# Performance work log

Measured on AMD Instinct MI355X. Metric: run time of the kernel, lower is better.

The kernel has to match this reference:

```python
import jax, jax.numpy as jnp
import numpy as np

N_HEADS = 16
SCALE = 0.25  # hard-coded in the torch module


def setup_inputs() -> dict:
    key = jax.random.key(0)
    ks = jax.random.split(key, 5)
    B, S, D = 2, 2048, 1024
    std = 1.0 / np.sqrt(D)
    return {
        "x": jax.random.normal(ks[0], (B, S, D), dtype=jnp.float32),
        "wq": jax.random.normal(ks[1], (D, D), dtype=jnp.float32) * std,
        "wk": jax.random.normal(ks[2], (D, D), dtype=jnp.float32) * std,
        "wv": jax.random.normal(ks[3], (D, D), dtype=jnp.float32) * std,
        "wo": jax.random.normal(ks[4], (D, D), dtype=jnp.float32) * std,
    }


def reference(x, wq, wk, wv, wo):
    B, S, D = x.shape
    H = N_HEADS
    hd = D // H
    # torch Linear(no bias): y = x @ W.T ; weights stored [out, in]
    q = (x @ wq.T).reshape(B, S, H, hd).transpose(0, 2, 1, 3)  # [B,H,S,hd]
    k = (x @ wk.T).reshape(B, S, H, hd).transpose(0, 2, 1, 3)
    v = (x @ wv.T).reshape(B, S, H, hd).transpose(0, 2, 1, 3)

    scores = jnp.einsum("bhqd,bhkd->bhqk", q, k) * SCALE  # [B,H,S,S]
    idx = jnp.arange(S)
    q_idx = idx[:, None]
    kv_idx = idx[None, :]
    # ALiBi-style score_mod: score - |q_idx - kv_idx|
    bias = -jnp.abs(q_idx - kv_idx).astype(scores.dtype)  # [S,S]
    causal = q_idx >= kv_idx  # [S,S]
    scores = jnp.where(causal, scores + bias, -jnp.inf)
    attn = jax.nn.softmax(scores, axis=-1)
    out = jnp.einsum("bhqk,bhkd->bhqd", attn, v)  # [B,H,S,hd]
    out = out.transpose(0, 2, 1, 3).reshape(B, S, D)
    return out @ wo.T
```

## Files before the change

kernel.cpp:

```cpp
#include <hip/hip_runtime.h>
#include <hip/hip_bf16.h>
#include <stdint.h>

typedef __bf16 bf16x8 __attribute__((ext_vector_type(8)));
typedef __bf16 bf16x4 __attribute__((ext_vector_type(4)));
typedef float  f32x4  __attribute__((ext_vector_type(4)));
typedef uint32_t u32x4 __attribute__((ext_vector_type(4)));

#define LOG2E 1.44269504088896f

__device__ __forceinline__ void glds16(const __bf16* g, __bf16* l) {
  __builtin_amdgcn_global_load_lds((const __attribute__((address_space(1))) void*)g,
                                   (__attribute__((address_space(3))) void*)l, 16, 0, 0);
}

__device__ __forceinline__ uint32_t pk2(float lo, float hi) {
  __bf16 l = (__bf16)lo, h = (__bf16)hi;
  uint16_t lb = __builtin_bit_cast(uint16_t, l);
  uint16_t hb = __builtin_bit_cast(uint16_t, h);
  return ((uint32_t)hb << 16) | lb;
}

__global__ __launch_bounds__(256) void cvt_all(
    const float* __restrict__ x,  const float* __restrict__ wq,
    const float* __restrict__ wk, const float* __restrict__ wv,
    const float* __restrict__ wo,
    __bf16* __restrict__ xb,  __bf16* __restrict__ wqb,
    __bf16* __restrict__ wkb, __bf16* __restrict__ wvb,
    __bf16* __restrict__ wob) {
  int i = blockIdx.x * 256 + threadIdx.x;
  const float* src; __bf16* dst; int j;
  if (i < 1048576) { src = x; dst = xb; j = i; }
  else {
    int t = i - 1048576;
    int w = t >> 18;
    j = t & 262143;
    src = (w == 0) ? wq : (w == 1) ? wk : (w == 2) ? wv : wo;
    dst = (w == 0) ? wqb : (w == 1) ? wkb : (w == 2) ? wvb : wob;
  }
  float4 v = ((const float4*)src)[j];
  bf16x4 o = { (__bf16)v.x, (__bf16)v.y, (__bf16)v.z, (__bf16)v.w };
  ((bf16x4*)dst)[j] = o;
}


__global__ __launch_bounds__(256, 3)
void qkv_gemm(const __bf16* __restrict__ A,
              const __bf16* __restrict__ Wq, const __bf16* __restrict__ Wk,
              const __bf16* __restrict__ Wv,
              __bf16* __restrict__ Qo, __bf16* __restrict__ Ko,
              __bf16* __restrict__ Vo) {
  __shared__ __bf16 As[3][128 * 32];
  __shared__ __bf16 Bs[3][128 * 32];
  const int tid  = threadIdx.x;
  const int lane = tid & 63;
  const int wv   = tid >> 6;
  const int l15  = lane & 15, lg = lane >> 4;
  const int wr   = (wv >> 1) << 6;
  const int wc   = (wv & 1) << 6;
  const int which = blockIdx.x >> 3;
  const __bf16* W = (which == 0) ? Wq : (which == 1) ? Wk : Wv;
  const long rowBase = (long)blockIdx.y * 128;
  const long colBase = (long)(blockIdx.x & 7) * 128;

  const __bf16* aSrc[2]; const __bf16* bSrc[2]; int ldsOff[2];
#pragma unroll
  for (int i = 0; i < 2; ++i) {
    int c = i * 256 + tid;
    int row = c >> 2;
    int lc = ((c & 3) - (row >> 1)) & 3;
    aSrc[i] = A + (rowBase + row) * 1024 + lc * 8;
    bSrc[i] = W + (colBase + row) * 1024 + lc * 8;
    ldsOff[i] = c * 8;
  }
  int aOff[4], bOff[4];
#pragma unroll
  for (int t = 0; t < 4; ++t) {
    int rA = wr + t * 16 + l15;
    int rB = wc + t * 16 + l15;
    aOff[t] = rA * 32 + (((lg + (rA >> 1)) & 3) << 3);
    bOff[t] = rB * 32 + (((lg + (rB >> 1)) & 3) << 3);
  }

  f32x4 acc[4][4] = {};
#pragma unroll
  for (int i = 0; i < 2; ++i) {
    glds16(aSrc[i], &As[0][ldsOff[i]]);
    glds16(bSrc[i], &Bs[0][ldsOff[i]]);
  }
#pragma unroll
  for (int i = 0; i < 2; ++i) {
    glds16(aSrc[i] + 32, &As[1][ldsOff[i]]);
    glds16(bSrc[i] + 32, &Bs[1][ldsOff[i]]);
  }
  asm volatile("s_waitcnt vmcnt(4)" ::: "memory");
  __builtin_amdgcn_s_barrier();
  __builtin_amdgcn_sched_barrier(0);

  int cur = 0;
  for (int kt = 0; kt < 32; ++kt) {
    bf16x8 af[4], bfr[4];
#pragma unroll
    for (int t = 0; t < 4; ++t) {
      af[t]  = *(const bf16x8*)(&As[cur][aOff[t]]);
      bfr[t] = *(const bf16x8*)(&Bs[cur][bOff[t]]);
    }
    if (kt < 30) {
      int nb = cur + 2; if (nb >= 3) nb -= 3;
      const int k2 = (kt + 2) << 5;
#pragma unroll
      for (int i = 0; i < 2; ++i) {
        glds16(aSrc[i] + k2, &As[nb][ldsOff[i]]);
        glds16(bSrc[i] + k2, &Bs[nb][ldsOff[i]]);
      }
    }
    __builtin_amdgcn_s_setprio(1);
#pragma unroll
    for (int mi = 0; mi < 4; ++mi)
#pragma unroll
      for (int ni = 0; ni < 4; ++ni)
        acc[mi][ni] = __builtin_amdgcn_mfma_f32_16x16x32_bf16(af[mi], bfr[ni], acc[mi][ni], 0, 0, 0);
    __builtin_amdgcn_s_setprio(0);
    if (kt < 31) {
      if (kt < 30) asm volatile("s_waitcnt vmcnt(4)" ::: "memory");
      else         asm volatile("s_waitcnt vmcnt(0)" ::: "memory");
      __builtin_amdgcn_s_barrier();
      __builtin_amdgcn_sched_barrier(0);
    }
    cur += 1; if (cur >= 3) cur -= 3;
  }

  __bf16* dstp = (which == 0) ? Qo : Ko;
#pragma unroll
  for (int mi = 0; mi < 4; ++mi)
#pragma unroll
    for (int ni = 0; ni < 4; ++ni) {
      if (which == 2) {
        long row = rowBase + wr + mi * 16 + (lg << 2);
        long col = colBase + wc + ni * 16 + l15;
        long idx = ((row >> 11) * 1024 + col) * 2048 + (row & 2047);
        bf16x4 o = { (__bf16)acc[mi][ni][0], (__bf16)acc[mi][ni][1],
                     (__bf16)acc[mi][ni][2], (__bf16)acc[mi][ni][3] };
        *(bf16x4*)(&Vo[idx]) = o;
      } else {
#pragma unroll
        for (int r = 0; r < 4; ++r) {
          long row = rowBase + wr + mi * 16 + (lg << 2) + r;
          long col = colBase + wc + ni * 16 + l15;
          dstp[row * 1024 + col] = (__bf16)acc[mi][ni][r];
        }
      }
    }
}

__global__ __launch_bounds__(256, 2)
void wo_gemm(const __bf16* __restrict__ A, const __bf16* __restrict__ W,
             float* __restrict__ C) {
  __shared__ __bf16 As[3][64 * 32];
  __shared__ __bf16 Bs[3][128 * 32];
  const int tid  = threadIdx.x;
  const int lane = tid & 63;
  const int wv   = tid >> 6;
  const int l15  = lane & 15, lg = lane >> 4;
  const int wc   = wv << 5;
  const long rowBase = (long)blockIdx.y * 64;
  const long colBase = (long)blockIdx.x * 128;

  int arow = tid >> 2;
  int alc = ((tid & 3) - (arow >> 1)) & 3;
  const __bf16* aSrc = A + (rowBase + arow) * 1024 + alc * 8;
  int aOffL = tid * 8;
  const __bf16* bSrc[2]; int bOffL[2];
#pragma unroll
  for (int i = 0; i < 2; ++i) {
    int c = i * 256 + tid;
    int row = c >> 2;
    int lc = ((c & 3) - (row >> 1)) & 3;
    bSrc[i] = W + (colBase + row) * 1024 + lc * 8;
    bOffL[i] = c * 8;
  }
  int aOff[4], bOff[2];
#pragma unroll
  for (int t = 0; t < 4; ++t) {
    int rA = t * 16 + l15;
    aOff[t] = rA * 32 + (((lg + (rA >> 1)) & 3) << 3);
  }
#pragma unroll
  for (int n = 0; n < 2; ++n) {
    int rB = wc + n * 16 + l15;
    bOff[n] = rB * 32 + (((lg + (rB >> 1)) & 3) << 3);
  }

  f32x4 acc[4][2] = {};
  glds16(aSrc, &As[0][aOffL]);
#pragma unroll
  for (int i = 0; i < 2; ++i) glds16(bSrc[i], &Bs[0][bOffL[i]]);
  glds16(aSrc + 32, &As[1][aOffL]);
#pragma unroll
  for (int i = 0; i < 2; ++i) glds16(bSrc[i] + 32, &Bs[1][bOffL[i]]);
  asm volatile("s_waitcnt vmcnt(3)" ::: "memory");
  __builtin_amdgcn_s_barrier();
  __builtin_amdgcn_sched_barrier(0);

  int cur = 0;
  for (int kt = 0; kt < 32; ++kt) {
    bf16x8 af[4], bfr[2];
#pragma unroll
    for (int t = 0; t < 4; ++t) af[t] = *(const bf16x8*)(&As[cur][aOff[t]]);
#pragma unroll
    for (int n = 0; n < 2; ++n) bfr[n] = *(const bf16x8*)(&Bs[cur][bOff[n]]);
    if (kt < 30) {
      int nb = cur + 2; if (nb >= 3) nb -= 3;
      const int k2 = (kt + 2) << 5;
      glds16(aSrc + k2, &As[nb][aOffL]);
#pragma unroll
      for (int i = 0; i < 2; ++i) glds16(bSrc[i] + k2, &Bs[nb][bOffL[i]]);
    }
    __builtin_amdgcn_s_setprio(1);
#pragma unroll
    for (int mi = 0; mi < 4; ++mi)
#pragma unroll
      for (int ni = 0; ni < 2; ++ni)
        acc[mi][ni] = __builtin_amdgcn_mfma_f32_16x16x32_bf16(af[mi], bfr[ni], acc[mi][ni], 0, 0, 0);
    __builtin_amdgcn_s_setprio(0);
    if (kt < 31) {
      if (kt < 30) asm volatile("s_waitcnt vmcnt(3)" ::: "memory");
      else         asm volatile("s_waitcnt vmcnt(0)" ::: "memory");
      __builtin_amdgcn_s_barrier();
      __builtin_amdgcn_sched_barrier(0);
    }
    cur += 1; if (cur >= 3) cur -= 3;
  }

#pragma unroll
  for (int mi = 0; mi < 4; ++mi)
#pragma unroll
    for (int ni = 0; ni < 2; ++ni)
#pragma unroll
      for (int r = 0; r < 4; ++r) {
        long row = rowBase + mi * 16 + (lg << 2) + r;
        long col = colBase + wc + ni * 16 + l15;
        C[row * 1024 + col] = acc[mi][ni][r];
      }
}

#define LOADK(kv, dst)                                                         \
  dst[0] = *(const bf16x8*)(Kb + (long)((kv) + l15) * D + lg * 8);             \
  dst[1] = *(const bf16x8*)(Kb + (long)((kv) + l15) * D + 32 + lg * 8);        \
  dst[2] = *(const bf16x8*)(Kb + (long)((kv) + 16 + l15) * D + lg * 8);        \
  dst[3] = *(const bf16x8*)(Kb + (long)((kv) + 16 + l15) * D + 32 + lg * 8);
#define LOADV(kv, dst)                                                         \
  _Pragma("unroll")                                                            \
  for (int dg = 0; dg < 4; ++dg)                                               \
    dst[dg] = *(const bf16x8*)(Vb + (long)(dg * 16 + l15) * S + (kv) + lg * 8);

__global__ __launch_bounds__(256, 2)
void attn64(const __bf16* __restrict__ Q, const __bf16* __restrict__ Kk,
            const __bf16* __restrict__ VT, __bf16* __restrict__ O) {
  constexpr int S = 2048, D = 1024;
  constexpr float C0 = 0.25f * LOG2E;
  constexpr float FM = 14.0f;
  const int lane = threadIdx.x & 63;
  const int wv   = threadIdx.x >> 6;
  const int q0   = blockIdx.x * 128 + wv * 32;
  const int h = blockIdx.y, b = blockIdx.z;
  const __bf16* Qb = Q  + (long)b * S * D + h * 64;
  const __bf16* Kb = Kk + (long)b * S * D + h * 64;
  const __bf16* Vb = VT + (long)(b * 16 + h) * 64 * S;
  const int l15 = lane & 15, lg = lane >> 4;

  bf16x8 qf[2][2];
#pragma unroll
  for (int g = 0; g < 2; ++g) {
    qf[g][0] = *(const bf16x8*)(Qb + (long)(q0 + 16 * g + l15) * D + lg * 8);
    qf[g][1] = *(const bf16x8*)(Qb + (long)(q0 + 16 * g + l15) * D + 32 + lg * 8);
  }

  f32x4 acc[2][4] = {};
  float lsum[2] = {0.f, 0.f};

  const int srcA = l15 + ((lane & 16) ? 32 : 0);
  const int srcB = srcA + 16;
  const bool hi  = (lg >= 2);

  int kvb = (q0 > 192) ? ((q0 - 192) & ~31) : 0;
  bf16x8 ck[4], cv[4], nk[4], nv[4];
  LOADK(kvb, ck); LOADV(kvb, cv);

  for (; kvb <= q0; kvb += 32) {
    const bool more = (kvb + 32 <= q0);
    if (more) { LOADK(kvb + 32, nk); LOADV(kvb + 32, nv); }

    f32x4 sa[2], sb[2];
    __builtin_amdgcn_s_setprio(1);
#pragma unroll
    for (int g = 0; g < 2; ++g) {
      f32x4 za = {}, zb = {};
      za = __builtin_amdgcn_mfma_f32_16x16x32_bf16(ck[0], qf[g][0], za, 0, 0, 0);
      za = __builtin_amdgcn_mfma_f32_16x16x32_bf16(ck[1], qf[g][1], za, 0, 0, 0);
      zb = __builtin_amdgcn_mfma_f32_16x16x32_bf16(ck[2], qf[g][0], zb, 0, 0, 0);
      zb = __builtin_amdgcn_mfma_f32_16x16x32_bf16(ck[3], qf[g][1], zb, 0, 0, 0);
      sa[g] = za; sb[g] = zb;
    }
    __builtin_amdgcn_s_setprio(0);

    const bool diag = (kvb == q0);
#pragma unroll
    for (int g = 0; g < 2; ++g) {
      const int qg = q0 + 16 * g;
      float bL = ((float)(kvb + 4 * lg - qg - l15) - FM) * LOG2E;
      float ea[4], eb[4];
      if (!diag) {
#pragma unroll
        for (int r = 0; r < 4; ++r) {
          ea[r] = exp2f(fmaf(sa[g][r], C0, bL + (float)r * LOG2E));
          eb[r] = exp2f(fmaf(sb[g][r], C0, bL + (float)(r + 16) * LOG2E));
          lsum[g] += ea[r] + eb[r];
        }
      } else {
        int dc = l15 - 4 * lg;
#pragma unroll
        for (int r = 0; r < 4; ++r) {
          if (g == 0) {
            ea[r] = (r <= dc) ? exp2f(fmaf(sa[g][r], C0, bL + (float)r * LOG2E)) : 0.f;
            eb[r] = 0.f;
          } else {
            ea[r] = exp2f(fmaf(sa[g][r], C0, bL + (float)r * LOG2E));
            eb[r] = (r <= dc) ? exp2f(fmaf(sb[g][r], C0, bL + (float)(r + 16) * LOG2E)) : 0.f;
          }
          lsum[g] += ea[r] + eb[r];
        }
      }
      uint32_t wa0 = pk2(ea[0], ea[1]), wa1 = pk2(ea[2], ea[3]);
      uint32_t wb0 = pk2(eb[0], eb[1]), wb1 = pk2(eb[2], eb[3]);
      uint32_t a0 = __shfl(wa0, srcA), a1 = __shfl(wa1, srcA);
      uint32_t a2 = __shfl(wa0, srcB), a3 = __shfl(wa1, srcB);
      uint32_t b0 = __shfl(wb0, srcA), b1 = __shfl(wb1, srcA);
      uint32_t b2 = __shfl(wb0, srcB), b3 = __shfl(wb1, srcB);
      u32x4 wt = { hi ? b0 : a0, hi ? b1 : a1, hi ? b2 : a2, hi ? b3 : a3 };
      bf16x8 pf = __builtin_bit_cast(bf16x8, wt);

      __builtin_amdgcn_s_setprio(1);
#pragma unroll
      for (int dg = 0; dg < 4; ++dg)
        acc[g][dg] = __builtin_amdgcn_mfma_f32_16x16x32_bf16(cv[dg], pf, acc[g][dg], 0, 0, 0);
      __builtin_amdgcn_s_setprio(0);
    }

    if (more) {
#pragma unroll
      for (int i = 0; i < 4; ++i) { ck[i] = nk[i]; cv[i] = nv[i]; }
    }
  }

#pragma unroll
  for (int g = 0; g < 2; ++g) {
    float s = lsum[g];
    s += __shfl_xor(s, 16);
    s += __shfl_xor(s, 32);
    float inv = 1.0f / s;
    int row = q0 + 16 * g + l15;
#pragma unroll
    for (int dg = 0; dg < 4; ++dg) {
      bf16x4 o = { (__bf16)(acc[g][dg][0] * inv), (__bf16)(acc[g][dg][1] * inv),
                   (__bf16)(acc[g][dg][2] * inv), (__bf16)(acc[g][dg][3] * inv) };
      *(bf16x4*)(&O[((long)b * S + row) * D + h * 64 + dg * 16 + 4 * lg]) = o;
    }
  }
}

extern "C" void kernel_launch(void* const* d_in, const int* in_sizes, int n_in,
                              void* d_out, int out_size, void* d_ws, size_t ws_size,
                              hipStream_t stream) {
  const float* x  = (const float*)d_in[0];
  const float* wq = (const float*)d_in[1];
  const float* wk = (const float*)d_in[2];
  const float* wv = (const float*)d_in[3];
  const float* wo = (const float*)d_in[4];
  float* out = (float*)d_out;
  char* ws = (char*)d_ws;
  const long MB = 1 << 20;
  __bf16* xb  = (__bf16*)(ws + 0 * MB);
  __bf16* wqb = (__bf16*)(ws + 8 * MB);
  __bf16* wkb = (__bf16*)(ws + 10 * MB);
  __bf16* wvb = (__bf16*)(ws + 12 * MB);
  __bf16* wob = (__bf16*)(ws + 14 * MB);
  __bf16* Qb  = (__bf16*)(ws + 16 * MB);
  __bf16* Kb  = (__bf16*)(ws + 24 * MB);
  __bf16* VTb = (__bf16*)(ws + 32 * MB);
  __bf16* Ab  = (__bf16*)(ws + 40 * MB);

  cvt_all<<<8192, 256, 0, stream>>>(x, wq, wk, wv, wo, xb, wqb, wkb, wvb, wob);
  qkv_gemm<<<dim3(24, 32), 256, 0, stream>>>(xb, wqb, wkb, wvb, Qb, Kb, VTb);
  attn64<<<dim3(16, 16, 2), 256, 0, stream>>>(Qb, Kb, VTb, Ab);
  wo_gemm<<<dim3(8, 64), 256, 0, stream>>>(Ab, wob, out);
}
```

Measured before the change: 82.99 us.

## Widen QKV GEMM tile to 128x256 to increase B-operand reuse

```diff
diff --git a/kernel.cpp b/kernel.cpp
--- a/kernel.cpp
+++ b/kernel.cpp
@@ -44,85 +44,92 @@
 }
 
 
-__global__ __launch_bounds__(256, 3)
+__global__ __launch_bounds__(256, 2)
 void qkv_gemm(const __bf16* __restrict__ A,
               const __bf16* __restrict__ Wq, const __bf16* __restrict__ Wk,
               const __bf16* __restrict__ Wv,
               __bf16* __restrict__ Qo, __bf16* __restrict__ Ko,
               __bf16* __restrict__ Vo) {
   __shared__ __bf16 As[3][128 * 32];
-  __shared__ __bf16 Bs[3][128 * 32];
+  __shared__ __bf16 Bs[3][256 * 32];
   const int tid  = threadIdx.x;
   const int lane = tid & 63;
   const int wv   = tid >> 6;
   const int l15  = lane & 15, lg = lane >> 4;
   const int wr   = (wv >> 1) << 6;
-  const int wc   = (wv & 1) << 6;
-  const int which = blockIdx.x >> 3;
+  const int wc   = (wv & 1) << 7;
+  const int which = blockIdx.x >> 2;
   const __bf16* W = (which == 0) ? Wq : (which == 1) ? Wk : Wv;
   const long rowBase = (long)blockIdx.y * 128;
-  const long colBase = (long)(blockIdx.x & 7) * 128;
-
-  const __bf16* aSrc[2]; const __bf16* bSrc[2]; int ldsOff[2];
+  const long colBase = (long)(blockIdx.x & 3) * 256;
+
+  const __bf16* aSrc[2]; int aOffL[2];
 #pragma unroll
   for (int i = 0; i < 2; ++i) {
     int c = i * 256 + tid;
     int row = c >> 2;
     int lc = ((c & 3) - (row >> 1)) & 3;
     aSrc[i] = A + (rowBase + row) * 1024 + lc * 8;
+    aOffL[i] = c * 8;
+  }
+  const __bf16* bSrc[4]; int bOffL[4];
+#pragma unroll
+  for (int i = 0; i < 4; ++i) {
+    int c = i * 256 + tid;
+    int row = c >> 2;
+    int lc = ((c & 3) - (row >> 1)) & 3;
     bSrc[i] = W + (colBase + row) * 1024 + lc * 8;
-    ldsOff[i] = c * 8;
-  }
-  int aOff[4], bOff[4];
+    bOffL[i] = c * 8;
+  }
+  int aOff[4], bOff[8];
 #pragma unroll
   for (int t = 0; t < 4; ++t) {
     int rA = wr + t * 16 + l15;
-    int rB = wc + t * 16 + l15;
     aOff[t] = rA * 32 + (((lg + (rA >> 1)) & 3) << 3);
-    bOff[t] = rB * 32 + (((lg + (rB >> 1)) & 3) << 3);
-  }
-
-  f32x4 acc[4][4] = {};
-#pragma unroll
-  for (int i = 0; i < 2; ++i) {
-    glds16(aSrc[i], &As[0][ldsOff[i]]);
-    glds16(bSrc[i], &Bs[0][ldsOff[i]]);
-  }
-#pragma unroll
-  for (int i = 0; i < 2; ++i) {
-    glds16(aSrc[i] + 32, &As[1][ldsOff[i]]);
-    glds16(bSrc[i] + 32, &Bs[1][ldsOff[i]]);
-  }
-  asm volatile("s_waitcnt vmcnt(4)" ::: "memory");
+  }
+#pragma unroll
+  for (int n = 0; n < 8; ++n) {
+    int rB = wc + n * 16 + l15;
+    bOff[n] = rB * 32 + (((lg + (rB >> 1)) & 3) << 3);
+  }
+
+  f32x4 acc[4][8] = {};
+#pragma unroll
+  for (int i = 0; i < 2; ++i) glds16(aSrc[i], &As[0][aOffL[i]]);
+#pragma unroll
+  for (int i = 0; i < 4; ++i) glds16(bSrc[i], &Bs[0][bOffL[i]]);
+#pragma unroll
+  for (int i = 0; i < 2; ++i) glds16(aSrc[i] + 32, &As[1][aOffL[i]]);
+#pragma unroll
+  for (int i = 0; i < 4; ++i) glds16(bSrc[i] + 32, &Bs[1][bOffL[i]]);
+  asm volatile("s_waitcnt vmcnt(6)" ::: "memory");
   __builtin_amdgcn_s_barrier();
   __builtin_amdgcn_sched_barrier(0);
 
   int cur = 0;
   for (int kt = 0; kt < 32; ++kt) {
-    bf16x8 af[4], bfr[4];
-#pragma unroll
-    for (int t = 0; t < 4; ++t) {
-      af[t]  = *(const bf16x8*)(&As[cur][aOff[t]]);
-      bfr[t] = *(const bf16x8*)(&Bs[cur][bOff[t]]);
-    }
+    bf16x8 af[4], bfr[8];
+#pragma unroll
+    for (int t = 0; t < 4; ++t) af[t] = *(const bf16x8*)(&As[cur][aOff[t]]);
+#pragma unroll
+    for (int n = 0; n < 8; ++n) bfr[n] = *(const bf16x8*)(&Bs[cur][bOff[n]]);
     if (kt < 30) {
       int nb = cur + 2; if (nb >= 3) nb -= 3;
       const int k2 = (kt + 2) << 5;
 #pragma unroll
-      for (int i = 0; i < 2; ++i) {
-        glds16(aSrc[i] + k2, &As[nb][ldsOff[i]]);
-        glds16(bSrc[i] + k2, &Bs[nb][ldsOff[i]]);
-      }
+      for (int i = 0; i < 2; ++i) glds16(aSrc[i] + k2, &As[nb][aOffL[i]]);
+#pragma unroll
+      for (int i = 0; i < 4; ++i) glds16(bSrc[i] + k2, &Bs[nb][bOffL[i]]);
     }
     __builtin_amdgcn_s_setprio(1);
 #pragma unroll
     for (int mi = 0; mi < 4; ++mi)
 #pragma unroll
-      for (int ni = 0; ni < 4; ++ni)
+      for (int ni = 0; ni < 8; ++ni)
         acc[mi][ni] = __builtin_amdgcn_mfma_f32_16x16x32_bf16(af[mi], bfr[ni], acc[mi][ni], 0, 0, 0);
     __builtin_amdgcn_s_setprio(0);
     if (kt < 31) {
-      if (kt < 30) asm volatile("s_waitcnt vmcnt(4)" ::: "memory");
+      if (kt < 30) asm volatile("s_waitcnt vmcnt(6)" ::: "memory");
       else         asm volatile("s_waitcnt vmcnt(0)" ::: "memory");
       __builtin_amdgcn_s_barrier();
       __builtin_amdgcn_sched_barrier(0);
@@ -134,7 +141,7 @@
 #pragma unroll
   for (int mi = 0; mi < 4; ++mi)
 #pragma unroll
-    for (int ni = 0; ni < 4; ++ni) {
+    for (int ni = 0; ni < 8; ++ni) {
       if (which == 2) {
         long row = rowBase + wr + mi * 16 + (lg << 2);
         long col = colBase + wc + ni * 16 + l15;
@@ -391,7 +398,7 @@
   __bf16* Ab  = (__bf16*)(ws + 40 * MB);
 
   cvt_all<<<8192, 256, 0, stream>>>(x, wq, wk, wv, wo, xb, wqb, wkb, wvb, wob);
-  qkv_gemm<<<dim3(24, 32), 256, 0, stream>>>(xb, wqb, wkb, wvb, Qb, Kb, VTb);
+  qkv_gemm<<<dim3(12, 32), 256, 0, stream>>>(xb, wqb, wkb, wvb, Qb, Kb, VTb);
   attn64<<<dim3(16, 16, 2), 256, 0, stream>>>(Qb, Kb, VTb, Ab);
   wo_gemm<<<dim3(8, 64), 256, 0, stream>>>(Ab, wob, out);
 }
```

Measured after the change: 84.42 us. Within noise of the previous version (+1.7%).
